# Optimization experiments

Hardware: AMD Instinct MI355X
Metric: run time of the kernel (lower is better)

Reference implementation:

```python
import jax, jax.numpy as jnp
import numpy as np


def setup_inputs() -> dict:
    key = jax.random.key(0)
    B, K, N = 4096, 64, 256
    x = jax.random.normal(key, (B, K * N), dtype=jnp.float32)
    return {"x": x, "k": K, "n": N}


def reference(x, k, n):
    # y = eye(k).repeat_interleave(n, dim=0) -> [k*n, k], one-hot block matrix.
    # x @ y is exactly a segment-sum over contiguous blocks of n columns.
    B = x.shape[0]
    pred = x.reshape(B, k, n).sum(axis=-1)  # [B, k]
    y = jnp.repeat(jnp.eye(k, dtype=x.dtype), n, axis=0)  # [k*n, k]
    return (pred, y)
```

## Files before the change

### kernel.cpp

```cpp
#include <hip/hip_runtime.h>


constexpr int K = 64;
constexpr int N = 256;

__global__ __launch_bounds__(256) void seg_sum_kernel(const float4* __restrict__ x4,
                                                      float* __restrict__ pred) {
    const int lane = threadIdx.x & 63;
    const int wave = threadIdx.x >> 6;
    const long long out_idx = (long long)blockIdx.x * 4 + wave;

    float4 v = x4[out_idx * (N / 4) + lane];
    float s = (v.x + v.y) + (v.z + v.w);

    #pragma unroll
    for (int off = 32; off >= 1; off >>= 1)
        s += __shfl_down(s, off, 64);

    if (lane == 0) pred[out_idx] = s;
}

__global__ __launch_bounds__(256) void eye_rep_kernel(float4* __restrict__ y4) {
    const int i = blockIdx.x * blockDim.x + threadIdx.x;
    const int r = i >> 4;
    const int cb = (i & 15) << 2;
    const int hot = r >> 8;
    float4 v;
    v.x = (cb + 0 == hot) ? 1.0f : 0.0f;
    v.y = (cb + 1 == hot) ? 1.0f : 0.0f;
    v.z = (cb + 2 == hot) ? 1.0f : 0.0f;
    v.w = (cb + 3 == hot) ? 1.0f : 0.0f;
    y4[i] = v;
}

extern "C" void kernel_launch(void* const* d_in, const int* in_sizes, int n_in,
                              void* d_out, int out_size, void* d_ws, size_t ws_size,
                              hipStream_t stream) {
    const float* x = (const float*)d_in[0];
    float* out = (float*)d_out;

    const int B = in_sizes[0] / (K * N);
    float* pred = out;
    float* y = out + (size_t)B * K;

    seg_sum_kernel<<<(B * K) / 4, 256, 0, stream>>>(
        reinterpret_cast<const float4*>(x), pred);

    eye_rep_kernel<<<(K * N * K / 4) / 256, 256, 0, stream>>>(
        reinterpret_cast<float4*>(y));
}
```

Baseline: 51.38 us.

## Fuse segment-sum and eye-repeat kernels into one grid-stride persistent kernel

Merges the two launches into a single kernel with a fixed grid of 2048 blocks. Each wave loops over segments in grid-stride fashion, and afterward all threads write the one-hot matrix in grid-stride fashion. Loads and stores use nontemporal builtins so the streaming traffic does not pollute the cache. This removes one launch and the gap between kernels, at the cost of fewer waves in flight per segment and a serialized second phase inside each block.

New measurement: 53.20 us. +3.5%, slower.

```diff
diff --git a/kernel.cpp b/kernel.cpp
--- a/kernel.cpp
+++ b/kernel.cpp
@@ -1,36 +1,44 @@
 #include <hip/hip_runtime.h>
 
 
+typedef float f32x4 __attribute__((ext_vector_type(4)));
+
 constexpr int K = 64;
 constexpr int N = 256;
+constexpr int BLOCKS = 2048;
+constexpr int TPB = 256;
 
-__global__ __launch_bounds__(256) void seg_sum_kernel(const float4* __restrict__ x4,
-                                                      float* __restrict__ pred) {
+__global__ __launch_bounds__(TPB) void fused_kernel(const f32x4* __restrict__ x4,
+                                                    float* __restrict__ pred,
+                                                    f32x4* __restrict__ y4,
+                                                    int total_seg) {
     const int lane = threadIdx.x & 63;
     const int wave = threadIdx.x >> 6;
-    const long long out_idx = (long long)blockIdx.x * 4 + wave;
+    const int wave_stride = gridDim.x * (TPB / 64);
 
-    float4 v = x4[out_idx * (N / 4) + lane];
-    float s = (v.x + v.y) + (v.z + v.w);
+    for (long long seg = (long long)blockIdx.x * (TPB / 64) + wave;
+         seg < total_seg; seg += wave_stride) {
+        f32x4 v = __builtin_nontemporal_load(&x4[seg * (N / 4) + lane]);
+        float s = (v.x + v.y) + (v.z + v.w);
+        #pragma unroll
+        for (int off = 32; off >= 1; off >>= 1)
+            s += __shfl_down(s, off, 64);
+        if (lane == 0) __builtin_nontemporal_store(s, &pred[seg]);
+    }
 
-    #pragma unroll
-    for (int off = 32; off >= 1; off >>= 1)
-        s += __shfl_down(s, off, 64);
-
-    if (lane == 0) pred[out_idx] = s;
-}
-
-__global__ __launch_bounds__(256) void eye_rep_kernel(float4* __restrict__ y4) {
-    const int i = blockIdx.x * blockDim.x + threadIdx.x;
-    const int r = i >> 4;
-    const int cb = (i & 15) << 2;
-    const int hot = r >> 8;
-    float4 v;
-    v.x = (cb + 0 == hot) ? 1.0f : 0.0f;
-    v.y = (cb + 1 == hot) ? 1.0f : 0.0f;
-    v.z = (cb + 2 == hot) ? 1.0f : 0.0f;
-    v.w = (cb + 3 == hot) ? 1.0f : 0.0f;
-    y4[i] = v;
+    const int tid = blockIdx.x * TPB + threadIdx.x;
+    const int nthreads = gridDim.x * TPB;
+    for (int i = tid; i < (K * N * K) / 4; i += nthreads) {
+        const int r = i >> 4;
+        const int cb = (i & 15) << 2;
+        const int hot = r >> 8;
+        f32x4 v;
+        v.x = (cb + 0 == hot) ? 1.0f : 0.0f;
+        v.y = (cb + 1 == hot) ? 1.0f : 0.0f;
+        v.z = (cb + 2 == hot) ? 1.0f : 0.0f;
+        v.w = (cb + 3 == hot) ? 1.0f : 0.0f;
+        __builtin_nontemporal_store(v, &y4[i]);
+    }
 }
 
 extern "C" void kernel_launch(void* const* d_in, const int* in_sizes, int n_in,
@@ -40,12 +48,11 @@
     float* out = (float*)d_out;
 
     const int B = in_sizes[0] / (K * N);
+    const int total_seg = B * K;
     float* pred = out;
     float* y = out + (size_t)B * K;
 
-    seg_sum_kernel<<<(B * K) / 4, 256, 0, stream>>>(
-        reinterpret_cast<const float4*>(x), pred);
-
-    eye_rep_kernel<<<(K * N * K / 4) / 256, 256, 0, stream>>>(
-        reinterpret_cast<float4*>(y));
+    fused_kernel<<<BLOCKS, TPB, 0, stream>>>(
+        reinterpret_cast<const f32x4*>(x), pred,
+        reinterpret_cast<f32x4*>(y), total_seg);
 }
```
